# Optimization experiments

Measured on AMD Instinct MI355X. Metric: run time of the kernel, lower is better.

Reference implementation:

```python
import jax, jax.numpy as jnp
import numpy as np
import math

HIDDEN = 2048
HEADS = 16
GROUPS = 4
HEAD_DIM = HIDDEN // HEADS  # 128
KV_DIM = GROUPS * HEAD_DIM  # 512
B, S = 2, 2048


def setup_inputs() -> dict:
    key = jax.random.key(0)
    ks = jax.random.split(key, 10)
    scale = 0.02
    return {
        "X": jax.random.normal(ks[0], (B, S, HIDDEN), dtype=jnp.float32),
        "attention_mask": jnp.ones((B, S), dtype=jnp.int32),
        "Wq": jax.random.normal(ks[1], (HIDDEN, HIDDEN), dtype=jnp.float32) * scale,
        "bq": jnp.zeros((HIDDEN,), dtype=jnp.float32),
        "Wk": jax.random.normal(ks[2], (HIDDEN, KV_DIM), dtype=jnp.float32) * scale,
        "bk": jnp.zeros((KV_DIM,), dtype=jnp.float32),
        "Wv": jax.random.normal(ks[3], (HIDDEN, KV_DIM), dtype=jnp.float32) * scale,
        "bv": jnp.zeros((KV_DIM,), dtype=jnp.float32),
        "Wo": jax.random.normal(ks[4], (HIDDEN, HIDDEN), dtype=jnp.float32) * scale,
        "bo": jnp.zeros((HIDDEN,), dtype=jnp.float32),
    }


def reference(X, attention_mask, Wq, bq, Wk, bk, Wv, bv, Wo, bo):
    b, s, _ = X.shape
    num_per_group = HEADS // GROUPS
    # projections
    Q = (X @ Wq + bq).reshape(b, s, HEADS, HEAD_DIM).transpose(0, 2, 1, 3)   # [b,H,s,d]
    K = (X @ Wk + bk).reshape(b, s, GROUPS, HEAD_DIM).transpose(0, 2, 1, 3)  # [b,G,s,d]
    V = (X @ Wv + bv).reshape(b, s, GROUPS, HEAD_DIM).transpose(0, 2, 1, 3)
    # torch .repeat(1, num_per_group, 1, 1) tiles group axis: [g0..gG-1, g0..gG-1, ...]
    K = jnp.tile(K, (1, num_per_group, 1, 1))  # [b,H,s,d]
    V = jnp.tile(V, (1, num_per_group, 1, 1))
    scores = jnp.einsum("bhqd,bhkd->bhqk", Q, K) / math.sqrt(HEAD_DIM)
    mask = attention_mask[:, None, None, :] == 0  # [b,1,1,s]
    scores = jnp.where(mask, jnp.float32(-jnp.inf), scores)
    attn = jax.nn.softmax(scores, axis=-1)
    out = jnp.einsum("bhqk,bhkd->bhqd", attn, V)  # [b,H,s,d]
    out = out.transpose(0, 2, 1, 3).reshape(b, s, HIDDEN)
    return out @ Wo + bo
```

## Files before the change

kernel.cpp:

```cpp
#include <hip/hip_runtime.h>
#include <hip/hip_bf16.h>


typedef __attribute__((ext_vector_type(8))) short short8;
typedef __attribute__((ext_vector_type(4))) short short4v;
typedef __attribute__((ext_vector_type(4))) float float4v;
typedef __attribute__((ext_vector_type(16))) float float16v;

#define C1F 0.12751743f
#define B0F -16.0f

#if defined(__has_builtin) && __has_builtin(__builtin_amdgcn_exp2f)
#define EXP2(x) __builtin_amdgcn_exp2f(x)
#else
#define EXP2(x) exp2f(x)
#endif

__device__ __forceinline__ short f2bf(float x) {
    __hip_bfloat16 h = __float2bfloat16(x);
    short s; __builtin_memcpy(&s, &h, sizeof(s)); return s;
}

__device__ __forceinline__ void gl16(const short* g, short* l) {
    __builtin_amdgcn_global_load_lds(
        (const __attribute__((address_space(1))) void*)g,
        (__attribute__((address_space(3))) void*)l, 16, 0, 0);
}

__global__ __launch_bounds__(256) void cvt_bf16_kernel(const float* __restrict__ in,
                                                       short* __restrict__ out, int n) {
    int i = (blockIdx.x * 256 + threadIdx.x) * 4;
    if (i >= n) return;
    float4 v = *(const float4*)(in + i);
    short4v o;
    o[0] = f2bf(v.x); o[1] = f2bf(v.y); o[2] = f2bf(v.z); o[3] = f2bf(v.w);
    *(short4v*)(out + i) = o;
}

__global__ __launch_bounds__(256) void transpose_all_kernel(
    const float* __restrict__ Wq, const float* __restrict__ Wk,
    const float* __restrict__ Wv, const float* __restrict__ Wo,
    short* __restrict__ WqkvT, short* __restrict__ Wot) {
    __shared__ float tile[32][33];
    int bx = blockIdx.x;
    const float* W; short* Wt; int N;
    if (bx < 64)      { W = Wq; Wt = WqkvT;                      N = 2048; }
    else if (bx < 80) { W = Wk; Wt = WqkvT + (size_t)2048 * 2048; N = 512; bx -= 64; }
    else if (bx < 96) { W = Wv; Wt = WqkvT + (size_t)2560 * 2048; N = 512; bx -= 80; }
    else              { W = Wo; Wt = Wot;                        N = 2048; bx -= 96; }
    const int K = 2048;
    int n0 = bx * 32, k0 = blockIdx.y * 32;
    int tx = threadIdx.x & 31, ty = threadIdx.x >> 5;
#pragma unroll
    for (int i = 0; i < 4; ++i) {
        int kk = ty + i * 8;
        tile[kk][tx] = W[(size_t)(k0 + kk) * N + n0 + tx];
    }
    __syncthreads();
#pragma unroll
    for (int i = 0; i < 4; ++i) {
        int nn = ty + i * 8;
        Wt[(size_t)(n0 + nn) * K + k0 + tx] = f2bf(tile[tx][nn]);
    }
}

__global__ __launch_bounds__(256) void gemm_dma_kernel(
    const short* __restrict__ A, const short* __restrict__ Bt,
    const float* __restrict__ b0, const float* __restrict__ b1, const float* __restrict__ b2,
    short* __restrict__ O0, short* __restrict__ O1, short* __restrict__ O2,
    float* __restrict__ Of, int K, int mode) {
    __shared__ short As[128 * 32];
    __shared__ short Bs[128 * 32];
    const int t = threadIdx.x, lane = t & 63, w = t >> 6;
    const int l15 = lane & 15, quad = lane >> 4;
    const int wm = (w & 1) * 64, wn = (w >> 1) * 64;
    const int m0 = blockIdx.y * 128, n0 = blockIdx.x * 128;
    const int r4 = lane >> 2, c8 = (lane & 3) * 8;
    const short* ga = A + (size_t)(m0 + w * 16 + r4) * K + c8;
    const short* gb = Bt + (size_t)(n0 + w * 16 + r4) * K + c8;
    short* lA = As + (w * 16) * 32;
    short* lB = Bs + (w * 16) * 32;

    float4v acc[4][4] = {};

    for (int k0 = 0; k0 < K; k0 += 32) {
        gl16(ga + k0, lA);
        gl16(ga + (size_t)64 * K + k0, lA + 64 * 32);
        gl16(gb + k0, lB);
        gl16(gb + (size_t)64 * K + k0, lB + 64 * 32);
        __syncthreads();
        short8 af[4], bfr[4];
#pragma unroll
        for (int i = 0; i < 4; ++i)
            af[i] = *(const short8*)(As + (wm + i * 16 + l15) * 32 + quad * 8);
#pragma unroll
        for (int j = 0; j < 4; ++j)
            bfr[j] = *(const short8*)(Bs + (wn + j * 16 + l15) * 32 + quad * 8);
#pragma unroll
        for (int i = 0; i < 4; ++i)
#pragma unroll
            for (int j = 0; j < 4; ++j)
                acc[i][j] = __builtin_amdgcn_mfma_f32_16x16x32_bf16(af[i], bfr[j], acc[i][j], 0, 0, 0);
        __syncthreads();
    }

#pragma unroll
    for (int i = 0; i < 4; ++i) {
#pragma unroll
        for (int j = 0; j < 4; ++j) {
            const int col = n0 + wn + j * 16 + l15;
            const int row0 = m0 + wm + i * 16 + quad * 4;
            if (mode == 1) {
                const float bc = b0[col];
#pragma unroll
                for (int r = 0; r < 4; ++r)
                    Of[(size_t)(row0 + r) * 2048 + col] = acc[i][j][r] + bc;
            } else if (col < 2048) {
                const float bc = b0[col];
#pragma unroll
                for (int r = 0; r < 4; ++r)
                    O0[(size_t)(row0 + r) * 2048 + col] = f2bf(acc[i][j][r] + bc);
            } else if (col < 2560) {
                const int c = col - 2048;
                const float bc = b1[c];
#pragma unroll
                for (int r = 0; r < 4; ++r)
                    O1[(size_t)(row0 + r) * 512 + c] = f2bf(acc[i][j][r] + bc);
            } else {
                const int c = col - 2560;
                const float bc = b2[c];
                const int qsw = ((quad & 1) << 1) | (quad >> 1);
                const int prow = m0 + wm + i * 16 + qsw * 4;
#pragma unroll
                for (int r = 0; r < 4; ++r)
                    O2[(size_t)c * 4096 + prow + r] = f2bf(acc[i][j][r] + bc);
            }
        }
    }
}

__global__ __launch_bounds__(256, 2) void flash_kernel(
    const short* __restrict__ Qb, const short* __restrict__ Kb,
    const short* __restrict__ Vt, const int* __restrict__ mask,
    short* __restrict__ Ab) {
    __shared__ short Ks[2][64 * 136];
    __shared__ short Vs[2][128 * 72];

    const int t = threadIdx.x;
    const int lane = t & 63, w = t >> 6;
    const int l31 = lane & 31, hi = lane >> 5;
    const int qt = blockIdx.x, g = blockIdx.y, b = blockIdx.z;
    const int h = g + 4 * w;
    const int q0 = qt * 32;

    short8 qf[8];
#pragma unroll
    for (int dd = 0; dd < 8; ++dd)
        qf[dd] = *(const short8*)(Qb + (size_t)(b * 2048 + q0 + l31) * 2048
                                  + h * 128 + dd * 16 + hi * 8);

    float16v o[4] = {};
    float rsum = 0.f;

    const int kR = t >> 4, kC = (t & 15) * 8;
    const int vR = t >> 3, vC = (t & 7) * 8;
    const short* kg = Kb + (size_t)(b * 2048 + kR) * 512 + g * 128 + kC;
    const short* vg = Vt + (size_t)(g * 128 + vR) * 4096 + (size_t)b * 2048 + vC;

    short8 kv[4], vv[4];
    int mvr = 1;

#define LOADT(KB)                                                                  \
    do {                                                                           \
        kv[0] = *(const short8*)(kg + (size_t)(KB) * 512);                         \
        kv[1] = *(const short8*)(kg + (size_t)((KB) + 16) * 512);                  \
        kv[2] = *(const short8*)(kg + (size_t)((KB) + 32) * 512);                  \
        kv[3] = *(const short8*)(kg + (size_t)((KB) + 48) * 512);                  \
        vv[0] = *(const short8*)(vg + (KB));                                       \
        vv[1] = *(const short8*)(vg + (size_t)32 * 4096 + (KB));                   \
        vv[2] = *(const short8*)(vg + (size_t)64 * 4096 + (KB));                   \
        vv[3] = *(const short8*)(vg + (size_t)96 * 4096 + (KB));                   \
        mvr = mask[b * 2048 + (KB) + lane];                                        \
    } while (0)

#define STAGE(BUF)                                                                 \
    do {                                                                           \
        _Pragma("unroll")                                                          \
        for (int i_ = 0; i_ < 4; ++i_)                                             \
            *(short8*)(&Ks[BUF][(kR + i_ * 16) * 136 + kC]) = kv[i_];              \
        _Pragma("unroll")                                                          \
        for (int i_ = 0; i_ < 4; ++i_)                                             \
            *(short8*)(&Vs[BUF][(vR + i_ * 32) * 72 + vC]) = vv[i_];               \
    } while (0)

    LOADT(0);
    STAGE(0);
    unsigned long long bits = __ballot(mvr != 0);
    LOADT(64);
    __syncthreads();

    int cur = 0;
    unsigned long long bits_next = bits;

    for (int kt = 0; kt < 32; ++kt) {
        if (kt + 1 < 32) {
            STAGE(cur ^ 1);
            bits_next = __ballot(mvr != 0);
            if (kt + 2 < 32) LOADT((kt + 2) * 64);
        }
        const short* Ksb = &Ks[cur][0];
        const short* Vsb = &Vs[cur][0];

        float16v st0 = {}, st1 = {};
        __builtin_amdgcn_s_setprio(1);
#pragma unroll
        for (int dd = 0; dd < 8; ++dd) {
            short8 kf0 = *(const short8*)(Ksb + l31 * 136 + dd * 16 + hi * 8);
            short8 kf1 = *(const short8*)(Ksb + (32 + l31) * 136 + dd * 16 + hi * 8);
            st0 = __builtin_amdgcn_mfma_f32_32x32x16_bf16(kf0, qf[dd], st0, 0, 0, 0);
            st1 = __builtin_amdgcn_mfma_f32_32x32x16_bf16(kf1, qf[dd], st1, 0, 0, 0);
        }
        __builtin_amdgcn_s_setprio(0);

        const bool full = (bits == ~0ull);
        const unsigned int mlo = ((unsigned int)bits) >> (4 * hi);
        const unsigned int mhi = ((unsigned int)(bits >> 32)) >> (4 * hi);

        if (full) {
#pragma unroll
            for (int e = 0; e < 16; ++e) {
                float p0 = EXP2(fmaf(st0[e], C1F, B0F));
                rsum += p0; st0[e] = p0;
            }
        } else {
#pragma unroll
            for (int e = 0; e < 16; ++e) {
                const int koff = (e & 3) + 8 * (e >> 2);
                float p0 = EXP2(fmaf(st0[e], C1F, B0F));
                p0 = ((mlo >> koff) & 1) ? p0 : 0.f;
                rsum += p0; st0[e] = p0;
            }
        }

        __builtin_amdgcn_s_setprio(1);
#pragma unroll
        for (int cc = 0; cc < 2; ++cc) {
            short8 pa;
#pragma unroll
            for (int e = 0; e < 8; ++e) pa[e] = f2bf(st0[cc * 8 + e]);
#pragma unroll
            for (int db = 0; db < 4; ++db) {
                short8 vb = *(const short8*)(Vsb + (db * 32 + l31) * 72 + cc * 16 + hi * 8);
                o[db] = __builtin_amdgcn_mfma_f32_32x32x16_bf16(pa, vb, o[db], 0, 0, 0);
            }
        }
        __builtin_amdgcn_s_setprio(0);

        if (full) {
#pragma unroll
            for (int e = 0; e < 16; ++e) {
                float p1 = EXP2(fmaf(st1[e], C1F, B0F));
                rsum += p1; st1[e] = p1;
            }
        } else {
#pragma unroll
            for (int e = 0; e < 16; ++e) {
                const int koff = (e & 3) + 8 * (e >> 2);
                float p1 = EXP2(fmaf(st1[e], C1F, B0F));
                p1 = ((mhi >> koff) & 1) ? p1 : 0.f;
                rsum += p1; st1[e] = p1;
            }
        }

        __builtin_amdgcn_s_setprio(1);
#pragma unroll
        for (int cc = 2; cc < 4; ++cc) {
            short8 pa;
#pragma unroll
            for (int e = 0; e < 8; ++e) pa[e] = f2bf(st1[(cc & 1) * 8 + e]);
#pragma unroll
            for (int db = 0; db < 4; ++db) {
                short8 vb = *(const short8*)(Vsb + (db * 32 + l31) * 72 + cc * 16 + hi * 8);
                o[db] = __builtin_amdgcn_mfma_f32_32x32x16_bf16(pa, vb, o[db], 0, 0, 0);
            }
        }
        __builtin_amdgcn_s_setprio(0);

        __syncthreads();
        bits = bits_next;
        cur ^= 1;
    }
#undef LOADT
#undef STAGE

    rsum += __shfl_xor(rsum, 32, 64);
    const float rinv = (rsum > 0.f) ? 1.f / rsum : 0.f;
    float rq[16];
#pragma unroll
    for (int e = 0; e < 16; ++e) {
        const int koff = (e & 3) + 8 * (e >> 2);
        rq[e] = __shfl(rinv, koff + 4 * hi, 64);
    }
    const size_t ob = (size_t)(b * 2048 + q0) * 2048 + h * 128;
#pragma unroll
    for (int db = 0; db < 4; ++db)
#pragma unroll
        for (int e = 0; e < 16; ++e) {
            const int koff = (e & 3) + 8 * (e >> 2);
            Ab[ob + (size_t)(koff + 4 * hi) * 2048 + db * 32 + l31] =
                f2bf(o[db][e] * rq[e]);
        }
}

extern "C" void kernel_launch(void* const* d_in, const int* in_sizes, int n_in,
                              void* d_out, int out_size, void* d_ws, size_t ws_size,
                              hipStream_t stream) {
    (void)in_sizes; (void)n_in; (void)out_size; (void)ws_size;
    const float* X  = (const float*)d_in[0];
    const int* mask = (const int*)d_in[1];
    const float* Wq = (const float*)d_in[2];
    const float* bq = (const float*)d_in[3];
    const float* Wk = (const float*)d_in[4];
    const float* bk = (const float*)d_in[5];
    const float* Wv = (const float*)d_in[6];
    const float* bv = (const float*)d_in[7];
    const float* Wo = (const float*)d_in[8];
    const float* bo = (const float*)d_in[9];
    float* out = (float*)d_out;

    char* ws = (char*)d_ws;
    short* Xb     = (short*)(ws + 0);
    short* WqkvT  = (short*)(ws + 16777216);
    short* Wot    = (short*)(ws + 29360128);
    short* Qb     = (short*)(ws + 37748736);
    short* Kb     = (short*)(ws + 54525952);
    short* Vt     = (short*)(ws + 58720256);
    short* Ab     = Xb;

    const int M = 4096, HID = 2048;

    cvt_bf16_kernel<<<8192, 256, 0, stream>>>(X, Xb, M * HID);
    transpose_all_kernel<<<dim3(160, 64), 256, 0, stream>>>(Wq, Wk, Wv, Wo, WqkvT, Wot);

    gemm_dma_kernel<<<dim3(24, 32), 256, 0, stream>>>(
        Xb, WqkvT, bq, bk, bv, Qb, Kb, Vt, nullptr, HID, 0);

    flash_kernel<<<dim3(64, 4, 2), 256, 0, stream>>>(Qb, Kb, Vt, mask, Ab);

    gemm_dma_kernel<<<dim3(16, 32), 256, 0, stream>>>(
        Ab, Wot, bo, nullptr, nullptr, nullptr, nullptr, nullptr, out, HID, 1);
}
```

Baseline: 333.1 us.

## Replace GEMM with 256x256-tile double-buffered kernel using swizzled LDS and phased MFMA

Both projection GEMMs move from 128x128 tiles with a single LDS buffer and K-step 32 to 256x256 tiles with 512 threads and K-step 64. LDS is double-buffered, and the next tile's global-to-LDS loads are issued between MFMA phases. Reads use an XOR-swizzled LDS layout, and s_setprio plus barriers interleave the loads with the four MFMA quadrants. The aim is more data reuse per loaded byte and load latency hidden behind compute. The cost is far fewer blocks (192 and 128) on a 256-CU device, and large LDS use that limits occupancy.

```diff
diff --git a/kernel.cpp b/kernel.cpp
--- a/kernel.cpp
+++ b/kernel.cpp
@@ -64,76 +64,143 @@
     }
 }
 
-__global__ __launch_bounds__(256) void gemm_dma_kernel(
+__global__ __launch_bounds__(512, 2) void gemm256_kernel(
     const short* __restrict__ A, const short* __restrict__ Bt,
     const float* __restrict__ b0, const float* __restrict__ b1, const float* __restrict__ b2,
     short* __restrict__ O0, short* __restrict__ O1, short* __restrict__ O2,
     float* __restrict__ Of, int K, int mode) {
-    __shared__ short As[128 * 32];
-    __shared__ short Bs[128 * 32];
+    __shared__ short AL[2][256 * 64];
+    __shared__ short BL[2][256 * 64];
     const int t = threadIdx.x, lane = t & 63, w = t >> 6;
-    const int l15 = lane & 15, quad = lane >> 4;
-    const int wm = (w & 1) * 64, wn = (w >> 1) * 64;
-    const int m0 = blockIdx.y * 128, n0 = blockIdx.x * 128;
-    const int r4 = lane >> 2, c8 = (lane & 3) * 8;
-    const short* ga = A + (size_t)(m0 + w * 16 + r4) * K + c8;
-    const short* gb = Bt + (size_t)(n0 + w * 16 + r4) * K + c8;
-    short* lA = As + (w * 16) * 32;
-    short* lB = Bs + (w * 16) * 32;
-
-    float4v acc[4][4] = {};
-
-    for (int k0 = 0; k0 < K; k0 += 32) {
-        gl16(ga + k0, lA);
-        gl16(ga + (size_t)64 * K + k0, lA + 64 * 32);
-        gl16(gb + k0, lB);
-        gl16(gb + (size_t)64 * K + k0, lB + 64 * 32);
+    const int l15 = lane & 15, quad = (lane >> 4) & 3;
+    const int wr = w >> 2, wc = w & 3;
+    const int m0 = blockIdx.y * 256, n0 = blockIdx.x * 256;
+
+    const int srow = w * 8 + (lane >> 3);
+    const int scol = ((lane & 7) * 8) ^ ((lane >> 5) << 4);
+    const short* gA = A + (size_t)(m0 + srow) * K + scol;
+    const short* gB = Bt + (size_t)(n0 + srow) * K + scol;
+
+    float4v acc[8][4] = {};
+    const int NT = K >> 6;
+
+#define LDA4(DST, RBASE)                                                           \
+    _Pragma("unroll")                                                              \
+    for (int mi = 0; mi < 4; ++mi) {                                               \
+        const int row = (RBASE) + mi * 16 + l15;                                   \
+        const int cs = ((l15 >> 2) & 1) << 4;                                      \
+        _Pragma("unroll")                                                          \
+        for (int ks = 0; ks < 2; ++ks)                                             \
+            DST[mi][ks] = *(const short8*)(Abuf + row * 64 + ((ks * 32 + quad * 8) ^ cs)); \
+    }
+#define LDB2(NJ0)                                                                  \
+    _Pragma("unroll")                                                              \
+    for (int nj = 0; nj < 2; ++nj) {                                               \
+        const int row = wc * 64 + ((NJ0) + nj) * 16 + l15;                         \
+        const int cs = ((l15 >> 2) & 1) << 4;                                      \
+        _Pragma("unroll")                                                          \
+        for (int ks = 0; ks < 2; ++ks)                                             \
+            bf[(NJ0) + nj][ks] = *(const short8*)(Bbuf + row * 64 + ((ks * 32 + quad * 8) ^ cs)); \
+    }
+#define MQ(AF, MIB, NJ0)                                                           \
+    _Pragma("unroll")                                                              \
+    for (int mi = 0; mi < 4; ++mi)                                                 \
+    _Pragma("unroll")                                                              \
+    for (int nj = 0; nj < 2; ++nj)                                                 \
+    _Pragma("unroll")                                                              \
+    for (int ks = 0; ks < 2; ++ks)                                                 \
+        acc[(MIB) + mi][(NJ0) + nj] = __builtin_amdgcn_mfma_f32_16x16x32_bf16(     \
+            AF[mi][ks], bf[(NJ0) + nj][ks], acc[(MIB) + mi][(NJ0) + nj], 0, 0, 0);
+
+#pragma unroll
+    for (int c = 0; c < 4; ++c) {
+        gl16(gA + (size_t)c * 64 * K, &AL[0][(c * 64 + w * 8) * 64]);
+        gl16(gB + (size_t)c * 64 * K, &BL[0][(c * 64 + w * 8) * 64]);
+    }
+
+    for (int kt = 0; kt < NT; ++kt) {
+        const int cur = kt & 1;
+        const short* Abuf = &AL[cur][0];
+        const short* Bbuf = &BL[cur][0];
+        const size_t knext = (size_t)(kt + 1) * 64;
+        const bool pre = (kt + 1 < NT);
+
         __syncthreads();
-        short8 af[4], bfr[4];
-#pragma unroll
-        for (int i = 0; i < 4; ++i)
-            af[i] = *(const short8*)(As + (wm + i * 16 + l15) * 32 + quad * 8);
-#pragma unroll
-        for (int j = 0; j < 4; ++j)
-            bfr[j] = *(const short8*)(Bs + (wn + j * 16 + l15) * 32 + quad * 8);
-#pragma unroll
-        for (int i = 0; i < 4; ++i)
-#pragma unroll
-            for (int j = 0; j < 4; ++j)
-                acc[i][j] = __builtin_amdgcn_mfma_f32_16x16x32_bf16(af[i], bfr[j], acc[i][j], 0, 0, 0);
-        __syncthreads();
-    }
-
-#pragma unroll
-    for (int i = 0; i < 4; ++i) {
-#pragma unroll
-        for (int j = 0; j < 4; ++j) {
-            const int col = n0 + wn + j * 16 + l15;
-            const int row0 = m0 + wm + i * 16 + quad * 4;
+
+        short8 afA[4][2], afB[4][2], bf[4][2];
+
+        LDA4(afA, wr * 128);
+        LDB2(0);
+        if (pre) {
+#pragma unroll
+            for (int c = 0; c < 4; ++c)
+                gl16(gA + knext + (size_t)c * 64 * K, &AL[cur ^ 1][(c * 64 + w * 8) * 64]);
+        }
+        __builtin_amdgcn_s_barrier();
+        __builtin_amdgcn_s_setprio(1);
+        MQ(afA, 0, 0);
+        __builtin_amdgcn_s_setprio(0);
+        __builtin_amdgcn_s_barrier();
+
+        LDB2(2);
+        if (pre) {
+#pragma unroll
+            for (int c = 0; c < 4; ++c)
+                gl16(gB + knext + (size_t)c * 64 * K, &BL[cur ^ 1][(c * 64 + w * 8) * 64]);
+        }
+        __builtin_amdgcn_s_barrier();
+        __builtin_amdgcn_s_setprio(1);
+        MQ(afA, 0, 2);
+        __builtin_amdgcn_s_setprio(0);
+        __builtin_amdgcn_s_barrier();
+
+        LDA4(afB, wr * 128 + 64);
+        __builtin_amdgcn_s_barrier();
+        __builtin_amdgcn_s_setprio(1);
+        MQ(afB, 4, 2);
+        __builtin_amdgcn_s_setprio(0);
+        __builtin_amdgcn_s_barrier();
+
+        __builtin_amdgcn_s_barrier();
+        __builtin_amdgcn_s_setprio(1);
+        MQ(afB, 4, 0);
+        __builtin_amdgcn_s_setprio(0);
+        __builtin_amdgcn_s_barrier();
+    }
+#undef LDA4
+#undef LDB2
+#undef MQ
+
+#pragma unroll
+    for (int mi = 0; mi < 8; ++mi) {
+#pragma unroll
+        for (int nj = 0; nj < 4; ++nj) {
+            const int col = n0 + wc * 64 + nj * 16 + l15;
+            const int row0 = m0 + wr * 128 + mi * 16 + quad * 4;
             if (mode == 1) {
                 const float bc = b0[col];
 #pragma unroll
                 for (int r = 0; r < 4; ++r)
-                    Of[(size_t)(row0 + r) * 2048 + col] = acc[i][j][r] + bc;
+                    Of[(size_t)(row0 + r) * 2048 + col] = acc[mi][nj][r] + bc;
             } else if (col < 2048) {
                 const float bc = b0[col];
 #pragma unroll
                 for (int r = 0; r < 4; ++r)
-                    O0[(size_t)(row0 + r) * 2048 + col] = f2bf(acc[i][j][r] + bc);
+                    O0[(size_t)(row0 + r) * 2048 + col] = f2bf(acc[mi][nj][r] + bc);
             } else if (col < 2560) {
                 const int c = col - 2048;
                 const float bc = b1[c];
 #pragma unroll
                 for (int r = 0; r < 4; ++r)
-                    O1[(size_t)(row0 + r) * 512 + c] = f2bf(acc[i][j][r] + bc);
+                    O1[(size_t)(row0 + r) * 512 + c] = f2bf(acc[mi][nj][r] + bc);
             } else {
                 const int c = col - 2560;
                 const float bc = b2[c];
                 const int qsw = ((quad & 1) << 1) | (quad >> 1);
-                const int prow = m0 + wm + i * 16 + qsw * 4;
+                const int prow = m0 + wr * 128 + mi * 16 + qsw * 4;
 #pragma unroll
                 for (int r = 0; r < 4; ++r)
-                    O2[(size_t)c * 4096 + prow + r] = f2bf(acc[i][j][r] + bc);
+                    O2[(size_t)c * 4096 + prow + r] = f2bf(acc[mi][nj][r] + bc);
             }
         }
     }
@@ -342,11 +409,11 @@
     cvt_bf16_kernel<<<8192, 256, 0, stream>>>(X, Xb, M * HID);
     transpose_all_kernel<<<dim3(160, 64), 256, 0, stream>>>(Wq, Wk, Wv, Wo, WqkvT, Wot);
 
-    gemm_dma_kernel<<<dim3(24, 32), 256, 0, stream>>>(
+    gemm256_kernel<<<dim3(12, 16), 512, 0, stream>>>(
         Xb, WqkvT, bq, bk, bv, Qb, Kb, Vt, nullptr, HID, 0);
 
     flash_kernel<<<dim3(64, 4, 2), 256, 0, stream>>>(Qb, Kb, Vt, mask, Ab);
 
-    gemm_dma_kernel<<<dim3(16, 32), 256, 0, stream>>>(
+    gemm256_kernel<<<dim3(8, 16), 512, 0, stream>>>(
         Ab, Wot, bo, nullptr, nullptr, nullptr, nullptr, nullptr, out, HID, 1);
 }
```

Result: slower. 342.8 us (+2.9%).

## Load V fragments directly from global into registers and merge prep kernels

Applied to the files above, without the earlier changes.

The flash kernel stops staging V tiles through shared memory. Each wave now loads its V MFMA operands straight from global memory into registers at the start of every key tile, which drops the V LDS buffers and their stores and reads. The FP32-to-BF16 conversion of X and the weight transpose kernels are merged into one launch, saving one kernel launch. The cost is that each wave separately fetches the same V data (redundant global/L2 traffic across the 4 waves), plus 16 extra vector registers, with less latency hiding than the old double-buffered prefetch.

```diff
diff --git a/kernel.cpp b/kernel.cpp
--- a/kernel.cpp
+++ b/kernel.cpp
@@ -27,30 +27,32 @@
         (__attribute__((address_space(3))) void*)l, 16, 0, 0);
 }
 
-__global__ __launch_bounds__(256) void cvt_bf16_kernel(const float* __restrict__ in,
-                                                       short* __restrict__ out, int n) {
-    int i = (blockIdx.x * 256 + threadIdx.x) * 4;
-    if (i >= n) return;
-    float4 v = *(const float4*)(in + i);
-    short4v o;
-    o[0] = f2bf(v.x); o[1] = f2bf(v.y); o[2] = f2bf(v.z); o[3] = f2bf(v.w);
-    *(short4v*)(out + i) = o;
-}
-
-__global__ __launch_bounds__(256) void transpose_all_kernel(
+__global__ __launch_bounds__(256) void prep_kernel(
+    const float* __restrict__ X, short* __restrict__ Xb,
     const float* __restrict__ Wq, const float* __restrict__ Wk,
     const float* __restrict__ Wv, const float* __restrict__ Wo,
     short* __restrict__ WqkvT, short* __restrict__ Wot) {
     __shared__ float tile[32][33];
-    int bx = blockIdx.x;
+    const int bxg = blockIdx.x;
+    if (bxg < 8192) {
+        int i = (bxg * 256 + threadIdx.x) * 4;
+        float4 v = *(const float4*)(X + i);
+        short4v o;
+        o[0] = f2bf(v.x); o[1] = f2bf(v.y); o[2] = f2bf(v.z); o[3] = f2bf(v.w);
+        *(short4v*)(Xb + i) = o;
+        return;
+    }
+    const int tid = bxg - 8192;
+    int bx = tid % 160;
+    const int k0 = (tid / 160) * 32;
     const float* W; short* Wt; int N;
     if (bx < 64)      { W = Wq; Wt = WqkvT;                      N = 2048; }
     else if (bx < 80) { W = Wk; Wt = WqkvT + (size_t)2048 * 2048; N = 512; bx -= 64; }
     else if (bx < 96) { W = Wv; Wt = WqkvT + (size_t)2560 * 2048; N = 512; bx -= 80; }
     else              { W = Wo; Wt = Wot;                        N = 2048; bx -= 96; }
     const int K = 2048;
-    int n0 = bx * 32, k0 = blockIdx.y * 32;
-    int tx = threadIdx.x & 31, ty = threadIdx.x >> 5;
+    const int n0 = bx * 32;
+    const int tx = threadIdx.x & 31, ty = threadIdx.x >> 5;
 #pragma unroll
     for (int i = 0; i < 4; ++i) {
         int kk = ty + i * 8;
@@ -144,7 +146,6 @@
     const short* __restrict__ Vt, const int* __restrict__ mask,
     short* __restrict__ Ab) {
     __shared__ short Ks[2][64 * 136];
-    __shared__ short Vs[2][128 * 72];
 
     const int t = threadIdx.x;
     const int lane = t & 63, w = t >> 6;
@@ -163,53 +164,53 @@
     float rsum = 0.f;
 
     const int kR = t >> 4, kC = (t & 15) * 8;
-    const int vR = t >> 3, vC = (t & 7) * 8;
     const short* kg = Kb + (size_t)(b * 2048 + kR) * 512 + g * 128 + kC;
-    const short* vg = Vt + (size_t)(g * 128 + vR) * 4096 + (size_t)b * 2048 + vC;
-
-    short8 kv[4], vv[4];
+    const short* vgw = Vt + (size_t)(g * 128 + l31) * 4096 + (size_t)b * 2048 + hi * 8;
+
+    short8 kv[4];
     int mvr = 1;
 
-#define LOADT(KB)                                                                  \
+#define LOADK(KB)                                                                  \
     do {                                                                           \
         kv[0] = *(const short8*)(kg + (size_t)(KB) * 512);                         \
         kv[1] = *(const short8*)(kg + (size_t)((KB) + 16) * 512);                  \
         kv[2] = *(const short8*)(kg + (size_t)((KB) + 32) * 512);                  \
         kv[3] = *(const short8*)(kg + (size_t)((KB) + 48) * 512);                  \
-        vv[0] = *(const short8*)(vg + (KB));                                       \
-        vv[1] = *(const short8*)(vg + (size_t)32 * 4096 + (KB));                   \
-        vv[2] = *(const short8*)(vg + (size_t)64 * 4096 + (KB));                   \
-        vv[3] = *(const short8*)(vg + (size_t)96 * 4096 + (KB));                   \
         mvr = mask[b * 2048 + (KB) + lane];                                        \
     } while (0)
 
-#define STAGE(BUF)                                                                 \
+#define STAGEK(BUF)                                                                \
     do {                                                                           \
         _Pragma("unroll")                                                          \
         for (int i_ = 0; i_ < 4; ++i_)                                             \
             *(short8*)(&Ks[BUF][(kR + i_ * 16) * 136 + kC]) = kv[i_];              \
-        _Pragma("unroll")                                                          \
-        for (int i_ = 0; i_ < 4; ++i_)                                             \
-            *(short8*)(&Vs[BUF][(vR + i_ * 32) * 72 + vC]) = vv[i_];               \
     } while (0)
 
-    LOADT(0);
-    STAGE(0);
+    LOADK(0);
+    STAGEK(0);
     unsigned long long bits = __ballot(mvr != 0);
-    LOADT(64);
+    LOADK(64);
     __syncthreads();
 
     int cur = 0;
     unsigned long long bits_next = bits;
 
     for (int kt = 0; kt < 32; ++kt) {
+        const int kb = kt * 64;
+
+        short8 vr[16];
+#pragma unroll
+        for (int cc = 0; cc < 4; ++cc)
+#pragma unroll
+            for (int db = 0; db < 4; ++db)
+                vr[cc * 4 + db] = *(const short8*)(vgw + (size_t)(db * 32) * 4096 + kb + cc * 16);
+
         if (kt + 1 < 32) {
-            STAGE(cur ^ 1);
+            STAGEK(cur ^ 1);
             bits_next = __ballot(mvr != 0);
-            if (kt + 2 < 32) LOADT((kt + 2) * 64);
+            if (kt + 2 < 32) LOADK((kt + 2) * 64);
         }
         const short* Ksb = &Ks[cur][0];
-        const short* Vsb = &Vs[cur][0];
 
         float16v st0 = {}, st1 = {};
         __builtin_amdgcn_s_setprio(1);
@@ -249,10 +250,8 @@
 #pragma unroll
             for (int e = 0; e < 8; ++e) pa[e] = f2bf(st0[cc * 8 + e]);
 #pragma unroll
-            for (int db = 0; db < 4; ++db) {
-                short8 vb = *(const short8*)(Vsb + (db * 32 + l31) * 72 + cc * 16 + hi * 8);
-                o[db] = __builtin_amdgcn_mfma_f32_32x32x16_bf16(pa, vb, o[db], 0, 0, 0);
-            }
+            for (int db = 0; db < 4; ++db)
+                o[db] = __builtin_amdgcn_mfma_f32_32x32x16_bf16(pa, vr[cc * 4 + db], o[db], 0, 0, 0);
         }
         __builtin_amdgcn_s_setprio(0);
 
@@ -279,10 +278,8 @@
 #pragma unroll
             for (int e = 0; e < 8; ++e) pa[e] = f2bf(st1[(cc & 1) * 8 + e]);
 #pragma unroll
-            for (int db = 0; db < 4; ++db) {
-                short8 vb = *(const short8*)(Vsb + (db * 32 + l31) * 72 + cc * 16 + hi * 8);
-                o[db] = __builtin_amdgcn_mfma_f32_32x32x16_bf16(pa, vb, o[db], 0, 0, 0);
-            }
+            for (int db = 0; db < 4; ++db)
+                o[db] = __builtin_amdgcn_mfma_f32_32x32x16_bf16(pa, vr[cc * 4 + db], o[db], 0, 0, 0);
         }
         __builtin_amdgcn_s_setprio(0);
 
@@ -290,8 +287,8 @@
         bits = bits_next;
         cur ^= 1;
     }
-#undef LOADT
-#undef STAGE
+#undef LOADK
+#undef STAGEK
 
     rsum += __shfl_xor(rsum, 32, 64);
     const float rinv = (rsum > 0.f) ? 1.f / rsum : 0.f;
@@ -337,10 +334,9 @@
     short* Vt     = (short*)(ws + 58720256);
     short* Ab     = Xb;
 
-    const int M = 4096, HID = 2048;
-
-    cvt_bf16_kernel<<<8192, 256, 0, stream>>>(X, Xb, M * HID);
-    transpose_all_kernel<<<dim3(160, 64), 256, 0, stream>>>(Wq, Wk, Wv, Wo, WqkvT, Wot);
+    const int HID = 2048;
+
+    prep_kernel<<<18432, 256, 0, stream>>>(X, Xb, Wq, Wk, Wv, Wo, WqkvT, Wot);
 
     gemm_dma_kernel<<<dim3(24, 32), 256, 0, stream>>>(
         Xb, WqkvT, bq, bk, bv, Qb, Kb, Vt, nullptr, HID, 0);
```

Result: slower. 393.0 us (+18.0%).

## Double GEMM K-tile to 64 with XOR-swizzled LDS and merge prep kernels

Applied to the files above, without the earlier changes.

The GEMM now loads a 64-wide K slice per iteration instead of 32. That halves the number of barrier pairs per K pass, and an XOR swizzle on the LDS column index is meant to avoid bank conflicts on the wider rows. Separately, the fp32->bf16 conversion of X and the weight transposes are merged into one launch, saving a kernel launch. The cost is doubled LDS use per block, which may reduce occupancy, and there is still no double buffering.

```diff
diff --git a/kernel.cpp b/kernel.cpp
--- a/kernel.cpp
+++ b/kernel.cpp
@@ -27,30 +27,32 @@
         (__attribute__((address_space(3))) void*)l, 16, 0, 0);
 }
 
-__global__ __launch_bounds__(256) void cvt_bf16_kernel(const float* __restrict__ in,
-                                                       short* __restrict__ out, int n) {
-    int i = (blockIdx.x * 256 + threadIdx.x) * 4;
-    if (i >= n) return;
-    float4 v = *(const float4*)(in + i);
-    short4v o;
-    o[0] = f2bf(v.x); o[1] = f2bf(v.y); o[2] = f2bf(v.z); o[3] = f2bf(v.w);
-    *(short4v*)(out + i) = o;
-}
-
-__global__ __launch_bounds__(256) void transpose_all_kernel(
+__global__ __launch_bounds__(256) void prep_kernel(
+    const float* __restrict__ X, short* __restrict__ Xb,
     const float* __restrict__ Wq, const float* __restrict__ Wk,
     const float* __restrict__ Wv, const float* __restrict__ Wo,
     short* __restrict__ WqkvT, short* __restrict__ Wot) {
     __shared__ float tile[32][33];
-    int bx = blockIdx.x;
+    const int bxg = blockIdx.x;
+    if (bxg < 8192) {
+        int i = (bxg * 256 + threadIdx.x) * 4;
+        float4 v = *(const float4*)(X + i);
+        short4v o;
+        o[0] = f2bf(v.x); o[1] = f2bf(v.y); o[2] = f2bf(v.z); o[3] = f2bf(v.w);
+        *(short4v*)(Xb + i) = o;
+        return;
+    }
+    const int tid = bxg - 8192;
+    int bx = tid % 160;
+    const int k0 = (tid / 160) * 32;
     const float* W; short* Wt; int N;
     if (bx < 64)      { W = Wq; Wt = WqkvT;                      N = 2048; }
     else if (bx < 80) { W = Wk; Wt = WqkvT + (size_t)2048 * 2048; N = 512; bx -= 64; }
     else if (bx < 96) { W = Wv; Wt = WqkvT + (size_t)2560 * 2048; N = 512; bx -= 80; }
     else              { W = Wo; Wt = Wot;                        N = 2048; bx -= 96; }
     const int K = 2048;
-    int n0 = bx * 32, k0 = blockIdx.y * 32;
-    int tx = threadIdx.x & 31, ty = threadIdx.x >> 5;
+    const int n0 = bx * 32;
+    const int tx = threadIdx.x & 31, ty = threadIdx.x >> 5;
 #pragma unroll
     for (int i = 0; i < 4; ++i) {
         int kk = ty + i * 8;
@@ -69,38 +71,45 @@
     const float* __restrict__ b0, const float* __restrict__ b1, const float* __restrict__ b2,
     short* __restrict__ O0, short* __restrict__ O1, short* __restrict__ O2,
     float* __restrict__ Of, int K, int mode) {
-    __shared__ short As[128 * 32];
-    __shared__ short Bs[128 * 32];
+    __shared__ short As[128 * 64];
+    __shared__ short Bs[128 * 64];
     const int t = threadIdx.x, lane = t & 63, w = t >> 6;
     const int l15 = lane & 15, quad = lane >> 4;
     const int wm = (w & 1) * 64, wn = (w >> 1) * 64;
     const int m0 = blockIdx.y * 128, n0 = blockIdx.x * 128;
-    const int r4 = lane >> 2, c8 = (lane & 3) * 8;
-    const short* ga = A + (size_t)(m0 + w * 16 + r4) * K + c8;
-    const short* gb = Bt + (size_t)(n0 + w * 16 + r4) * K + c8;
-    short* lA = As + (w * 16) * 32;
-    short* lB = Bs + (w * 16) * 32;
+    const int r8 = lane >> 3;
+    const int csw = ((lane & 7) ^ r8) * 8;
+    const short* ga = A + (size_t)(m0 + w * 8 + r8) * K + csw;
+    const short* gb = Bt + (size_t)(n0 + w * 8 + r8) * K + csw;
+    short* lA = As + (w * 8) * 64;
+    short* lB = Bs + (w * 8) * 64;
+    const int xs = l15 & 7;
 
     float4v acc[4][4] = {};
 
-    for (int k0 = 0; k0 < K; k0 += 32) {
-        gl16(ga + k0, lA);
-        gl16(ga + (size_t)64 * K + k0, lA + 64 * 32);
-        gl16(gb + k0, lB);
-        gl16(gb + (size_t)64 * K + k0, lB + 64 * 32);
+    for (int k0 = 0; k0 < K; k0 += 64) {
+#pragma unroll
+        for (int c = 0; c < 4; ++c) {
+            gl16(ga + k0 + (size_t)(c * 32) * K, lA + c * 2048);
+            gl16(gb + k0 + (size_t)(c * 32) * K, lB + c * 2048);
+        }
         __syncthreads();
-        short8 af[4], bfr[4];
-#pragma unroll
-        for (int i = 0; i < 4; ++i)
-            af[i] = *(const short8*)(As + (wm + i * 16 + l15) * 32 + quad * 8);
-#pragma unroll
-        for (int j = 0; j < 4; ++j)
-            bfr[j] = *(const short8*)(Bs + (wn + j * 16 + l15) * 32 + quad * 8);
-#pragma unroll
-        for (int i = 0; i < 4; ++i)
+#pragma unroll
+        for (int ks = 0; ks < 2; ++ks) {
+            short8 af[4], bfr[4];
+            const int ps = ((ks * 4 + quad) ^ xs) * 8;
+#pragma unroll
+            for (int i = 0; i < 4; ++i)
+                af[i] = *(const short8*)(As + (wm + i * 16 + l15) * 64 + ps);
 #pragma unroll
             for (int j = 0; j < 4; ++j)
-                acc[i][j] = __builtin_amdgcn_mfma_f32_16x16x32_bf16(af[i], bfr[j], acc[i][j], 0, 0, 0);
+                bfr[j] = *(const short8*)(Bs + (wn + j * 16 + l15) * 64 + ps);
+#pragma unroll
+            for (int i = 0; i < 4; ++i)
+#pragma unroll
+                for (int j = 0; j < 4; ++j)
+                    acc[i][j] = __builtin_amdgcn_mfma_f32_16x16x32_bf16(af[i], bfr[j], acc[i][j], 0, 0, 0);
+        }
         __syncthreads();
     }
 
@@ -337,10 +346,9 @@
     short* Vt     = (short*)(ws + 58720256);
     short* Ab     = Xb;
 
-    const int M = 4096, HID = 2048;
-
-    cvt_bf16_kernel<<<8192, 256, 0, stream>>>(X, Xb, M * HID);
-    transpose_all_kernel<<<dim3(160, 64), 256, 0, stream>>>(Wq, Wk, Wv, Wo, WqkvT, Wot);
+    const int HID = 2048;
+
+    prep_kernel<<<18432, 256, 0, stream>>>(X, Xb, Wq, Wk, Wv, Wo, WqkvT, Wot);
 
     gemm_dma_kernel<<<dim3(24, 32), 256, 0, stream>>>(
         Xb, WqkvT, bq, bk, bv, Qb, Kb, Vt, nullptr, HID, 0);
```

After: 304.8 us. 8.5% less time.
